# Kernel optimization log

Measured on AMD Instinct MI355X. Metric: run time of the kernel, lower is better.

Reference implementation:

```python
import jax, jax.numpy as jnp
import numpy as np

# DeformConv (RegSeg): offset conv + mask conv (sigmoid) + modulated deformable conv v2
STRIDE = 1
PAD = 1
DIL = 1
G = 1          # deformable_groups
KH, KW = 3, 3


def _conv(x, w, b):
    # standard NCHW conv, stride/pad/dilation of the module
    y = jax.lax.conv_general_dilated(
        x, w, window_strides=(STRIDE, STRIDE),
        padding=((PAD, PAD), (PAD, PAD)), rhs_dilation=(DIL, DIL),
        dimension_numbers=("NCHW", "OIHW", "NCHW"))
    return y + b[None, :, None, None]


def _deform_conv2d(x, offset, mask, w, b):
    # torchvision DeformConv2d (modulated, v2) semantics
    B, C, H, W = x.shape
    O = w.shape[0]
    K = KH * KW
    Ho = (H + 2 * PAD - DIL * (KH - 1) - 1) // STRIDE + 1
    Wo = (W + 2 * PAD - DIL * (KW - 1) - 1) // STRIDE + 1
    Cg = C // G

    # base sampling grid: p0 + p_k
    ky = jnp.repeat(jnp.arange(KH), KW) * DIL            # [K]
    kx = jnp.tile(jnp.arange(KW), KH) * DIL              # [K]
    oy = jnp.arange(Ho) * STRIDE - PAD                   # [Ho]
    ox = jnp.arange(Wo) * STRIDE - PAD                   # [Wo]
    base_y = (ky[:, None, None] + oy[None, :, None]).astype(x.dtype)  # [K,Ho,1]
    base_x = (kx[:, None, None] + ox[None, None, :]).astype(x.dtype)  # [K,1,Wo]

    off = offset.reshape(B, G, K, 2, Ho, Wo)             # channel layout: g, k, (dy,dx)
    py = base_y[None, None] + off[:, :, :, 0]            # [B,G,K,Ho,Wo]
    px = base_x[None, None] + off[:, :, :, 1]
    m = mask.reshape(B, G, K, Ho, Wo)

    imgf = x.reshape(B * G, Cg, H * W)
    y0 = jnp.floor(py).astype(jnp.int32)
    x0 = jnp.floor(px).astype(jnp.int32)
    ly = py - y0.astype(x.dtype)
    lx = px - x0.astype(x.dtype)

    def corner(iy, ix, wgt):
        # zero-padded bilinear corner: out-of-bounds corners contribute 0
        valid = (iy >= 0) & (iy < H) & (ix >= 0) & (ix < W)
        idx = (jnp.clip(iy, 0, H - 1) * W + jnp.clip(ix, 0, W - 1)).reshape(B * G, -1)
        g = jax.vmap(lambda im, ii: im[:, ii])(imgf, idx)            # [B*G,Cg,K*Ho*Wo]
        g = g.reshape(B, G, Cg, K, Ho, Wo)
        return g * (wgt * valid.astype(x.dtype))[:, :, None]          # [B,G,Cg,K,Ho,Wo]

    val = (corner(y0,     x0,     (1 - ly) * (1 - lx))
         + corner(y0,     x0 + 1, (1 - ly) * lx)
         + corner(y0 + 1, x0,     ly * (1 - lx))
         + corner(y0 + 1, x0 + 1, ly * lx))
    val = val * m[:, :, None]                                         # modulation

    wr = w.reshape(O, G, Cg, K)
    out = jnp.einsum("bgckpq,ogck->bopq", val, wr) + b[None, :, None, None]
    return out


def setup_inputs() -> dict:
    key = jax.random.key(0)
    ks = jax.random.split(key, 8)
    B, C, H, W, O = 4, 128, 96, 96, 128
    K = KH * KW
    fan = 1.0 / np.sqrt(C * K)
    return {
        "x":        jax.random.normal(ks[0], (B, C, H, W), jnp.float32),
        "x2":       jax.random.normal(ks[1], (B, C, H, W), jnp.float32),
        "offset_w": jax.random.normal(ks[2], (2 * G * K, C, KH, KW), jnp.float32) * 0.01,
        "offset_b": jax.random.normal(ks[3], (2 * G * K,), jnp.float32) * 0.01,
        "mask_w":   jax.random.normal(ks[4], (G * K, C, KH, KW), jnp.float32) * 0.05,
        "mask_b":   jnp.zeros((G * K,), jnp.float32),
        "deform_w": jax.random.normal(ks[5], (O, C, KH, KW), jnp.float32) * fan,
        "deform_b": jax.random.normal(ks[6], (O,), jnp.float32) * fan,
    }


def reference(x, x2, offset_w, offset_b, mask_w, mask_b, deform_w, deform_b):
    offset = _conv(x2, offset_w, offset_b)
    mask = jax.nn.sigmoid(_conv(x2, mask_w, mask_b))
    return _deform_conv2d(x, offset, mask, deform_w, deform_b)
```

## Files before the change

### kernel.cpp

```cpp
#include <hip/hip_runtime.h>

#define CIN   128
#define HH    96
#define WW    96
#define OUTC  128
#define HWSZ  9216
#define KK    9
#define KTOT  1152

typedef __bf16 bf16x8 __attribute__((ext_vector_type(8)));
typedef float  f32x4  __attribute__((ext_vector_type(4)));

__device__ __forceinline__ unsigned short f2bf(float f) {
  unsigned u = __builtin_bit_cast(unsigned, f);
  u += 0x7fffu + ((u >> 16) & 1u);
  return (unsigned short)(u >> 16);
}
__device__ __forceinline__ float bf2f_lo(unsigned w) {
  unsigned u = w << 16;
  return __builtin_bit_cast(float, u);
}
__device__ __forceinline__ float bf2f_hi(unsigned w) {
  unsigned u = w & 0xffff0000u;
  return __builtin_bit_cast(float, u);
}
__device__ __forceinline__ unsigned pack_bf(float v0, float v1) {
  unsigned u0 = __builtin_bit_cast(unsigned, v0) + 0x8000u;
  unsigned u1 = __builtin_bit_cast(unsigned, v1) + 0x8000u;
  return __builtin_amdgcn_perm(u1, u0, 0x07060302u);
}

#define WT2B_O 147456
#define BIAS_O 184320
#define XN_O   184384
#define X2N_O  (184384 + 4718592)

__global__ __launch_bounds__(256) void prep_all(
    const float* __restrict__ x, const float* __restrict__ x2,
    const float* __restrict__ offw, const float* __restrict__ maskw,
    const float* __restrict__ defw, const float* __restrict__ offb,
    const float* __restrict__ maskb, void* __restrict__ wsv) {
  int bid = blockIdx.x;
  int t = threadIdx.x;
  if (bid < 1152) {
    __shared__ unsigned short tile[64][138];
    int tsel = bid / 576;
    int rem = bid - tsel * 576;
    int b = rem / 144;
    int hw0 = (rem % 144) * 64;
    const float* src = tsel ? x2 : x;
    unsigned short* dst = (unsigned short*)wsv + (tsel ? X2N_O : XN_O);
    int px = t & 63, cg = t >> 6;
#pragma unroll
    for (int q = 0; q < 16; ++q) {
      int c = cg * 32 + 2 * q;
      float f0 = src[((size_t)(b * CIN + c))     * HWSZ + hw0 + px];
      float f1 = src[((size_t)(b * CIN + c + 1)) * HWSZ + hw0 + px];
      *(unsigned*)&tile[px][c] = pack_bf(f0, f1);
    }
    __syncthreads();
    unsigned* drow = (unsigned*)(dst + ((size_t)(b * HWSZ + hw0)) * 128);
#pragma unroll
    for (int k = 0; k < 16; ++k) {
      int e = t + 256 * k;
      int pxx = e >> 6, j = e & 63;
      unsigned v = *(const unsigned*)&tile[pxx][2 * j];
      drow[(size_t)pxx * 64 + j] = v;
    }
    return;
  }
  unsigned short* wtb  = (unsigned short*)wsv;
  unsigned short* wt2b = wtb + WT2B_O;
  float* bias32 = (float*)(wtb + BIAS_O);
  int idx = (bid - 1152) * 256 + t;
  if (idx < OUTC * KTOT) {
    int o = idx / KTOT, r = idx - o * KTOT;
    int c = r / KK, tap = r - c * KK;
    wtb[o * KTOT + tap * 128 + c] = f2bf(defw[idx]);
  } else if (idx < OUTC * KTOT + 32 * KTOT) {
    int j = idx - OUTC * KTOT;
    int oc = j / KTOT, r = j - oc * KTOT;
    int c = r / KK, tap = r - c * KK;
    float v = 0.f;
    if (oc < 18)      v = offw[j];
    else if (oc < 27) v = maskw[j - 18 * KTOT];
    wt2b[oc * KTOT + tap * 128 + c] = f2bf(v);
  } else if (idx < OUTC * KTOT + 32 * KTOT + 32) {
    int j = idx - OUTC * KTOT - 32 * KTOT;
    float v = 0.f;
    if (j < 18) v = offb[j]; else if (j < 27) v = maskb[j - 18];
    bias32[j] = v;
  }
}

__global__ __launch_bounds__(256, 3) void fused(
    const float* __restrict__ defb, const void* __restrict__ wsv,
    float* __restrict__ out) {
  const unsigned short* wtb  = (const unsigned short*)wsv;
  const unsigned short* wt2b = wtb + WT2B_O;
  const float* bias32 = (const float*)(wtb + BIAS_O);
  const unsigned short* xn  = wtb + XN_O;
  const unsigned short* x2n = wtb + X2N_O;

  __shared__ unsigned bw[64 * 68];
  __shared__ unsigned short val[64][136];
  __shared__ float om[32][68];
  __shared__ unsigned sidxw[KK * 4 * 64];

  int t = threadIdx.x;
  int w = t >> 6;
  int l15 = t & 15, quad = (t >> 4) & 3;
  int rb = blockIdx.x;
  int bid = (rb & 7) * 72 + (rb >> 3);
  int b = bid / 144;
  int pblk = (bid % 144) * 64;

  int phg[4], pwg[4];
#pragma unroll
  for (int G = 0; G < 4; ++G) {
    int p = pblk + w * 16 + G * 4 + quad;
    phg[G] = p / WW;
    pwg[G] = p - phg[G] * WW;
  }

  f32x4 oa0 = {0.f, 0.f, 0.f, 0.f};
  f32x4 oa1 = {0.f, 0.f, 0.f, 0.f};
  const unsigned short* x2nb = x2n + ((size_t)b * HWSZ) * 128;
  for (int tap = 0; tap < KK; ++tap) {
    int ky = tap / 3 - 1, kx = tap % 3 - 1;
    uint4 vG[4];
#pragma unroll
    for (int G = 0; G < 4; ++G) {
      int y = phg[G] + ky, xx = pwg[G] + kx;
      bool ok = ((unsigned)y < HH) && ((unsigned)xx < WW);
      int pos = ok ? (y * WW + xx) : 0;
      uint4 v = *(const uint4*)(x2nb + ((size_t)pos << 7) + l15 * 8);
      vG[G] = ok ? v : make_uint4(0u, 0u, 0u, 0u);
    }
#pragma unroll
    for (int j = 0; j < 2; ++j) {
      int cc = t + 256 * j;
      int row = cc >> 4, c16 = cc & 15;
      *(uint4*)&bw[row * 68 + c16 * 4] =
          *(const uint4*)(wt2b + (size_t)row * KTOT + tap * 128 + c16 * 8);
    }
#pragma unroll
    for (int G = 0; G < 4; ++G)
      *(uint4*)&val[w * 16 + G * 4 + quad][l15 * 8] = vG[G];
    __syncthreads();
#pragma unroll
    for (int ks = 0; ks < 4; ++ks) {
      bf16x8 af = *(const bf16x8*)&val[w * 16 + l15][ks * 32 + quad * 8];
      bf16x8 b0 = *(const bf16x8*)&bw[(size_t)l15 * 68 + ks * 16 + quad * 4];
      bf16x8 b1 = *(const bf16x8*)&bw[(size_t)(l15 + 16) * 68 + ks * 16 + quad * 4];
      oa0 = __builtin_amdgcn_mfma_f32_16x16x32_bf16(af, b0, oa0, 0, 0, 0);
      oa1 = __builtin_amdgcn_mfma_f32_16x16x32_bf16(af, b1, oa1, 0, 0, 0);
    }
    __syncthreads();
  }
#pragma unroll
  for (int nt = 0; nt < 2; ++nt) {
    f32x4 a = nt ? oa1 : oa0;
    int oc = nt * 16 + l15;
    float bia = bias32[oc];
#pragma unroll
    for (int r = 0; r < 4; ++r)
      om[oc][w * 16 + quad * 4 + r] = a[r] + bia;
  }
  __syncthreads();

  for (int e = t; e < KK * 64; e += 256) {
    int tap = e >> 6, pp = e & 63;
    int gp2 = pblk + pp;
    int h = gp2 / WW, ww_ = gp2 % WW;
    float dy = om[2 * tap][pp], dx = om[2 * tap + 1][pp];
    float mr = om[18 + tap][pp];
    float m = 1.f / (1.f + __expf(-mr));
    float py  = (float)(h + tap / 3 - 1) + dy;
    float pxx = (float)(ww_ + tap % 3 - 1) + dx;
    float y0f = floorf(py), x0f = floorf(pxx);
    int y0 = (int)y0f, x0 = (int)x0f;
    float ly = py - y0f, lx = pxx - x0f;
    int y1 = y0 + 1, x1 = x0 + 1;
    bool vy0 = (unsigned)y0 < HH, vy1 = (unsigned)y1 < HH;
    bool vx0 = (unsigned)x0 < WW, vx1 = (unsigned)x1 < WW;
    int cy0 = min(max(y0, 0), HH - 1), cy1 = min(max(y1, 0), HH - 1);
    int cx0 = min(max(x0, 0), WW - 1), cx1 = min(max(x1, 0), WW - 1);
    unsigned i00 = cy0 * WW + cx0, i01 = cy0 * WW + cx1;
    unsigned i10 = cy1 * WW + cx0, i11 = cy1 * WW + cx1;
    float w00 = (vy0 && vx0) ? m * (1.f - ly) * (1.f - lx) : 0.f;
    float w01 = (vy0 && vx1) ? m * (1.f - ly) * lx         : 0.f;
    float w10 = (vy1 && vx0) ? m * ly * (1.f - lx)         : 0.f;
    float w11 = (vy1 && vx1) ? m * ly * lx                 : 0.f;
    sidxw[(tap * 4 + 0) * 64 + pp] = i00 | ((unsigned)f2bf(w00) << 16);
    sidxw[(tap * 4 + 1) * 64 + pp] = i01 | ((unsigned)f2bf(w01) << 16);
    sidxw[(tap * 4 + 2) * 64 + pp] = i10 | ((unsigned)f2bf(w10) << 16);
    sidxw[(tap * 4 + 3) * 64 + pp] = i11 | ((unsigned)f2bf(w11) << 16);
  }
  __syncthreads();

  f32x4 acc[8];
#pragma unroll
  for (int nt = 0; nt < 8; ++nt) acc[nt] = (f32x4){0.f, 0.f, 0.f, 0.f};
  const unsigned short* xnb = xn + ((size_t)b * HWSZ) * 128;

  for (int tap = 0; tap < KK; ++tap) {
    unsigned sw[4][4];
#pragma unroll
    for (int cr = 0; cr < 4; ++cr)
#pragma unroll
      for (int G = 0; G < 4; ++G)
        sw[cr][G] = sidxw[(tap * 4 + cr) * 64 + w * 16 + G * 4 + quad];
    uint4 v[4][4];
#pragma unroll
    for (int G = 0; G < 4; ++G)
#pragma unroll
      for (int cr = 0; cr < 4; ++cr)
        v[cr][G] = *(const uint4*)(xnb + ((size_t)(sw[cr][G] & 0xffffu) << 7) + l15 * 8);
#pragma unroll
    for (int G = 0; G < 4; ++G) {
      float f[8];
#pragma unroll
      for (int j = 0; j < 8; ++j) f[j] = 0.f;
#pragma unroll
      for (int cr = 0; cr < 4; ++cr) {
        float wc = bf2f_hi(sw[cr][G]);
        const unsigned* a = (const unsigned*)&v[cr][G];
#pragma unroll
        for (int j = 0; j < 4; ++j) {
          f[2 * j]     += wc * bf2f_lo(a[j]);
          f[2 * j + 1] += wc * bf2f_hi(a[j]);
        }
      }
      unsigned od[4];
#pragma unroll
      for (int j = 0; j < 4; ++j) od[j] = pack_bf(f[2 * j], f[2 * j + 1]);
      *(uint4*)&val[w * 16 + G * 4 + quad][l15 * 8] =
          make_uint4(od[0], od[1], od[2], od[3]);
    }
#pragma unroll
    for (int j = 0; j < 4; ++j) {
      int cc = t + 256 * j;
      int row = cc >> 4, c16 = cc & 15;
      *(uint4*)&bw[row * 68 + c16 * 4] =
          *(const uint4*)(wtb + (size_t)row * KTOT + tap * 128 + c16 * 8);
    }
    __syncthreads();
    bf16x8 af[4];
#pragma unroll
    for (int ks = 0; ks < 4; ++ks)
      af[ks] = *(const bf16x8*)&val[w * 16 + l15][ks * 32 + quad * 8];
#pragma unroll
    for (int ks = 0; ks < 4; ++ks)
#pragma unroll
      for (int nt = 0; nt < 4; ++nt) {
        bf16x8 bb = *(const bf16x8*)&bw[(size_t)(nt * 16 + l15) * 68 + ks * 16 + quad * 4];
        acc[nt] = __builtin_amdgcn_mfma_f32_16x16x32_bf16(af[ks], bb, acc[nt], 0, 0, 0);
      }
    __syncthreads();
#pragma unroll
    for (int j = 0; j < 4; ++j) {
      int cc = t + 256 * j;
      int row = cc >> 4, c16 = cc & 15;
      *(uint4*)&bw[row * 68 + c16 * 4] =
          *(const uint4*)(wtb + (size_t)(64 + row) * KTOT + tap * 128 + c16 * 8);
    }
    __syncthreads();
#pragma unroll
    for (int ks = 0; ks < 4; ++ks)
#pragma unroll
      for (int nt = 0; nt < 4; ++nt) {
        bf16x8 bb = *(const bf16x8*)&bw[(size_t)(nt * 16 + l15) * 68 + ks * 16 + quad * 4];
        acc[4 + nt] = __builtin_amdgcn_mfma_f32_16x16x32_bf16(af[ks], bb, acc[4 + nt], 0, 0, 0);
      }
    __syncthreads();
  }

  for (int r = 0; r < 4; ++r) {
    f32x4 a0 = acc[2 * r], a1 = acc[2 * r + 1];
    float db0 = defb[r * 32 + l15];
    float db1 = defb[r * 32 + 16 + l15];
    if (r) __syncthreads();
#pragma unroll
    for (int reg = 0; reg < 4; ++reg) {
      om[l15]     [w * 16 + quad * 4 + reg] = a0[reg] + db0;
      om[16 + l15][w * 16 + quad * 4 + reg] = a1[reg] + db1;
    }
    __syncthreads();
    int row = t >> 4;
    int col4 = (t & 15) * 4;
#pragma unroll
    for (int hrow = 0; hrow < 2; ++hrow) {
      int rr = row + hrow * 16;
      float4 vv = *(float4*)&om[rr][col4];
      *(float4*)&out[((size_t)b * OUTC + r * 32 + rr) * HWSZ + pblk + col4] = vv;
    }
  }
}

extern "C" void kernel_launch(void* const* d_in, const int* in_sizes, int n_in,
                              void* d_out, int out_size, void* d_ws, size_t ws_size,
                              hipStream_t stream) {
  const float* x     = (const float*)d_in[0];
  const float* x2    = (const float*)d_in[1];
  const float* offw  = (const float*)d_in[2];
  const float* offb  = (const float*)d_in[3];
  const float* maskw = (const float*)d_in[4];
  const float* maskb = (const float*)d_in[5];
  const float* defw  = (const float*)d_in[6];
  const float* defb  = (const float*)d_in[7];
  float* out = (float*)d_out;

  hipLaunchKernelGGL(prep_all, dim3(1873), dim3(256), 0, stream,
                     x, x2, offw, maskw, defw, offb, maskb, d_ws);
  hipLaunchKernelGGL(fused, dim3(576), dim3(256), 0, stream, defb, d_ws, out);
}
```

Baseline: 143.7 us.

## Pipeline weight staging via global_load_lds and keep A fragments in registers

Both GEMM phases (offset/mask conv and deformable conv) are restructured. Each lane now loads its A-operand data directly in MFMA fragment layout into registers, which removes the LDS round-trip for activations. Weights are staged into a single swizzled 128x128 LDS buffer using direct global-to-LDS loads. A software pipeline issues the next tap's gathers before the current MFMAs, with manual vmcnt waits and barriers, so the output-channel halves no longer need separate passes. The hand-written waitcnt counts depend on the compiler's instruction ordering and could be fragile, and holding more data in registers may affect occupancy.

```diff
diff --git a/kernel.cpp b/kernel.cpp
--- a/kernel.cpp
+++ b/kernel.cpp
@@ -28,6 +28,11 @@
   unsigned u0 = __builtin_bit_cast(unsigned, v0) + 0x8000u;
   unsigned u1 = __builtin_bit_cast(unsigned, v1) + 0x8000u;
   return __builtin_amdgcn_perm(u1, u0, 0x07060302u);
+}
+__device__ __forceinline__ void gload16(const void* g, void* l) {
+  __builtin_amdgcn_global_load_lds(
+      (const __attribute__((address_space(1))) void*)g,
+      (__attribute__((address_space(3))) void*)l, 16, 0, 0);
 }
 
 #define WT2B_O 147456
@@ -102,8 +107,7 @@
   const unsigned short* xn  = wtb + XN_O;
   const unsigned short* x2n = wtb + X2N_O;
 
-  __shared__ unsigned bw[64 * 68];
-  __shared__ unsigned short val[64][136];
+  __shared__ unsigned short bwl[128 * 128];
   __shared__ float om[32][68];
   __shared__ unsigned sidxw[KK * 4 * 64];
 
@@ -115,49 +119,82 @@
   int b = bid / 144;
   int pblk = (bid % 144) * 64;
 
-  int phg[4], pwg[4];
-#pragma unroll
-  for (int G = 0; G < 4; ++G) {
-    int p = pblk + w * 16 + G * 4 + quad;
-    phg[G] = p / WW;
-    pwg[G] = p - phg[G] * WW;
-  }
-
+  int prow = pblk + w * 16 + l15;
+  int ph = prow / WW;
+  int pw_ = prow - ph * WW;
+
+  const unsigned short* x2nb = x2n + ((size_t)b * HWSZ) * 128;
+  const unsigned short* xnb  = xn  + ((size_t)b * HWSZ) * 128;
+
+  uint4 va[4]; unsigned okm;
+  auto issueA1 = [&](int tap) {
+    int ky = tap / 3 - 1, kx = tap % 3 - 1;
+    int y = ph + ky, xx = pw_ + kx;
+    bool ok = ((unsigned)y < HH) && ((unsigned)xx < WW);
+    int pos = ok ? (y * WW + xx) : 0;
+    const unsigned short* p = x2nb + ((size_t)pos << 7) + quad * 8;
+    va[0] = *(const uint4*)(p);
+    va[1] = *(const uint4*)(p + 32);
+    va[2] = *(const uint4*)(p + 64);
+    va[3] = *(const uint4*)(p + 96);
+    okm = ok ? 0xffffffffu : 0u;
+  };
+  auto maskA = [&](bf16x8* af) {
+#pragma unroll
+    for (int ks = 0; ks < 4; ++ks) {
+      uint4 m = va[ks];
+      m.x &= okm; m.y &= okm; m.z &= okm; m.w &= okm;
+      af[ks] = __builtin_bit_cast(bf16x8, m);
+    }
+  };
+  auto stage1 = [&](int tap) {
+#pragma unroll
+    for (int i = 0; i < 2; ++i) {
+      int r = (w * 2 + i) * 4 + quad;
+      const unsigned short* src =
+          wt2b + (size_t)r * KTOT + tap * 128 + ((l15 ^ (r & 7)) << 3);
+      gload16(src, (char*)bwl + ((w * 2 + i) << 10));
+    }
+  };
   f32x4 oa0 = {0.f, 0.f, 0.f, 0.f};
   f32x4 oa1 = {0.f, 0.f, 0.f, 0.f};
-  const unsigned short* x2nb = x2n + ((size_t)b * HWSZ) * 128;
-  for (int tap = 0; tap < KK; ++tap) {
-    int ky = tap / 3 - 1, kx = tap % 3 - 1;
-    uint4 vG[4];
-#pragma unroll
-    for (int G = 0; G < 4; ++G) {
-      int y = phg[G] + ky, xx = pwg[G] + kx;
-      bool ok = ((unsigned)y < HH) && ((unsigned)xx < WW);
-      int pos = ok ? (y * WW + xx) : 0;
-      uint4 v = *(const uint4*)(x2nb + ((size_t)pos << 7) + l15 * 8);
-      vG[G] = ok ? v : make_uint4(0u, 0u, 0u, 0u);
-    }
-#pragma unroll
-    for (int j = 0; j < 2; ++j) {
-      int cc = t + 256 * j;
-      int row = cc >> 4, c16 = cc & 15;
-      *(uint4*)&bw[row * 68 + c16 * 4] =
-          *(const uint4*)(wt2b + (size_t)row * KTOT + tap * 128 + c16 * 8);
-    }
-#pragma unroll
-    for (int G = 0; G < 4; ++G)
-      *(uint4*)&val[w * 16 + G * 4 + quad][l15 * 8] = vG[G];
-    __syncthreads();
+  auto mfma1 = [&](bf16x8* af) {
 #pragma unroll
     for (int ks = 0; ks < 4; ++ks) {
-      bf16x8 af = *(const bf16x8*)&val[w * 16 + l15][ks * 32 + quad * 8];
-      bf16x8 b0 = *(const bf16x8*)&bw[(size_t)l15 * 68 + ks * 16 + quad * 4];
-      bf16x8 b1 = *(const bf16x8*)&bw[(size_t)(l15 + 16) * 68 + ks * 16 + quad * 4];
-      oa0 = __builtin_amdgcn_mfma_f32_16x16x32_bf16(af, b0, oa0, 0, 0, 0);
-      oa1 = __builtin_amdgcn_mfma_f32_16x16x32_bf16(af, b1, oa1, 0, 0, 0);
-    }
-    __syncthreads();
-  }
+      int cs = ((ks * 4 + quad) ^ (l15 & 7)) << 4;
+      bf16x8 b0 = *(const bf16x8*)((const char*)bwl + l15 * 256 + cs);
+      bf16x8 b1 = *(const bf16x8*)((const char*)bwl + (l15 + 16) * 256 + cs);
+      oa0 = __builtin_amdgcn_mfma_f32_16x16x32_bf16(af[ks], b0, oa0, 0, 0, 0);
+      oa1 = __builtin_amdgcn_mfma_f32_16x16x32_bf16(af[ks], b1, oa1, 0, 0, 0);
+    }
+  };
+
+  issueA1(0);
+  asm volatile("" ::: "memory");
+  stage1(0);
+  asm volatile("" ::: "memory");
+#pragma unroll 1
+  for (int tap = 0; tap < 8; ++tap) {
+    bf16x8 af[4]; maskA(af);
+    issueA1(tap + 1);
+    asm volatile("s_waitcnt vmcnt(4)" ::: "memory");
+    __builtin_amdgcn_s_barrier();
+    asm volatile("" ::: "memory");
+    mfma1(af);
+    asm volatile("s_waitcnt lgkmcnt(0)" ::: "memory");
+    __builtin_amdgcn_s_barrier();
+    asm volatile("" ::: "memory");
+    stage1(tap + 1);
+    asm volatile("" ::: "memory");
+  }
+  {
+    bf16x8 af[4]; maskA(af);
+    asm volatile("s_waitcnt vmcnt(0)" ::: "memory");
+    __builtin_amdgcn_s_barrier();
+    asm volatile("" ::: "memory");
+    mfma1(af);
+  }
+
 #pragma unroll
   for (int nt = 0; nt < 2; ++nt) {
     f32x4 a = nt ? oa1 : oa0;
@@ -202,30 +239,32 @@
   f32x4 acc[8];
 #pragma unroll
   for (int nt = 0; nt < 8; ++nt) acc[nt] = (f32x4){0.f, 0.f, 0.f, 0.f};
-  const unsigned short* xnb = xn + ((size_t)b * HWSZ) * 128;
-
-  for (int tap = 0; tap < KK; ++tap) {
-    unsigned sw[4][4];
+
+  uint4 gv[4][4]; unsigned swv[4];
+  auto loadG = [&](int tap) {
 #pragma unroll
     for (int cr = 0; cr < 4; ++cr)
-#pragma unroll
-      for (int G = 0; G < 4; ++G)
-        sw[cr][G] = sidxw[(tap * 4 + cr) * 64 + w * 16 + G * 4 + quad];
-    uint4 v[4][4];
-#pragma unroll
-    for (int G = 0; G < 4; ++G)
-#pragma unroll
-      for (int cr = 0; cr < 4; ++cr)
-        v[cr][G] = *(const uint4*)(xnb + ((size_t)(sw[cr][G] & 0xffffu) << 7) + l15 * 8);
-#pragma unroll
-    for (int G = 0; G < 4; ++G) {
+      swv[cr] = sidxw[(tap * 4 + cr) * 64 + w * 16 + l15];
+#pragma unroll
+    for (int cr = 0; cr < 4; ++cr) {
+      const unsigned short* p =
+          xnb + ((size_t)(swv[cr] & 0xffffu) << 7) + quad * 8;
+      gv[cr][0] = *(const uint4*)(p);
+      gv[cr][1] = *(const uint4*)(p + 32);
+      gv[cr][2] = *(const uint4*)(p + 64);
+      gv[cr][3] = *(const uint4*)(p + 96);
+    }
+  };
+  auto combine = [&](bf16x8* af) {
+#pragma unroll
+    for (int ks = 0; ks < 4; ++ks) {
       float f[8];
 #pragma unroll
       for (int j = 0; j < 8; ++j) f[j] = 0.f;
 #pragma unroll
       for (int cr = 0; cr < 4; ++cr) {
-        float wc = bf2f_hi(sw[cr][G]);
-        const unsigned* a = (const unsigned*)&v[cr][G];
+        float wc = bf2f_hi(swv[cr]);
+        const unsigned* a = (const unsigned*)&gv[cr][ks];
 #pragma unroll
         for (int j = 0; j < 4; ++j) {
           f[2 * j]     += wc * bf2f_lo(a[j]);
@@ -235,45 +274,57 @@
       unsigned od[4];
 #pragma unroll
       for (int j = 0; j < 4; ++j) od[j] = pack_bf(f[2 * j], f[2 * j + 1]);
-      *(uint4*)&val[w * 16 + G * 4 + quad][l15 * 8] =
-          make_uint4(od[0], od[1], od[2], od[3]);
-    }
-#pragma unroll
-    for (int j = 0; j < 4; ++j) {
-      int cc = t + 256 * j;
-      int row = cc >> 4, c16 = cc & 15;
-      *(uint4*)&bw[row * 68 + c16 * 4] =
-          *(const uint4*)(wtb + (size_t)row * KTOT + tap * 128 + c16 * 8);
-    }
-    __syncthreads();
-    bf16x8 af[4];
-#pragma unroll
-    for (int ks = 0; ks < 4; ++ks)
-      af[ks] = *(const bf16x8*)&val[w * 16 + l15][ks * 32 + quad * 8];
-#pragma unroll
-    for (int ks = 0; ks < 4; ++ks)
-#pragma unroll
-      for (int nt = 0; nt < 4; ++nt) {
-        bf16x8 bb = *(const bf16x8*)&bw[(size_t)(nt * 16 + l15) * 68 + ks * 16 + quad * 4];
-        acc[nt] = __builtin_amdgcn_mfma_f32_16x16x32_bf16(af[ks], bb, acc[nt], 0, 0, 0);
+      uint4 u = make_uint4(od[0], od[1], od[2], od[3]);
+      af[ks] = __builtin_bit_cast(bf16x8, u);
+    }
+  };
+  auto stage3 = [&](int tap) {
+#pragma unroll
+    for (int i = 0; i < 8; ++i) {
+      int r = (w * 8 + i) * 4 + quad;
+      const unsigned short* src =
+          wtb + (size_t)r * KTOT + tap * 128 + ((l15 ^ (r & 7)) << 3);
+      gload16(src, (char*)bwl + ((w * 8 + i) << 10));
+    }
+  };
+  auto mfma3 = [&](bf16x8* af) {
+#pragma unroll
+    for (int ks = 0; ks < 4; ++ks) {
+      int cs = ((ks * 4 + quad) ^ (l15 & 7)) << 4;
+#pragma unroll
+      for (int nt = 0; nt < 8; ++nt) {
+        bf16x8 bb =
+            *(const bf16x8*)((const char*)bwl + (nt * 16 + l15) * 256 + cs);
+        acc[nt] = __builtin_amdgcn_mfma_f32_16x16x32_bf16(af[ks], bb, acc[nt],
+                                                          0, 0, 0);
       }
-    __syncthreads();
-#pragma unroll
-    for (int j = 0; j < 4; ++j) {
-      int cc = t + 256 * j;
-      int row = cc >> 4, c16 = cc & 15;
-      *(uint4*)&bw[row * 68 + c16 * 4] =
-          *(const uint4*)(wtb + (size_t)(64 + row) * KTOT + tap * 128 + c16 * 8);
-    }
-    __syncthreads();
-#pragma unroll
-    for (int ks = 0; ks < 4; ++ks)
-#pragma unroll
-      for (int nt = 0; nt < 4; ++nt) {
-        bf16x8 bb = *(const bf16x8*)&bw[(size_t)(nt * 16 + l15) * 68 + ks * 16 + quad * 4];
-        acc[4 + nt] = __builtin_amdgcn_mfma_f32_16x16x32_bf16(af[ks], bb, acc[4 + nt], 0, 0, 0);
-      }
-    __syncthreads();
+    }
+  };
+
+  loadG(0);
+  asm volatile("" ::: "memory");
+  stage3(0);
+  asm volatile("" ::: "memory");
+#pragma unroll 1
+  for (int tap = 0; tap < 8; ++tap) {
+    bf16x8 af[4]; combine(af);
+    loadG(tap + 1);
+    asm volatile("s_waitcnt vmcnt(16)" ::: "memory");
+    __builtin_amdgcn_s_barrier();
+    asm volatile("" ::: "memory");
+    mfma3(af);
+    asm volatile("s_waitcnt lgkmcnt(0)" ::: "memory");
+    __builtin_amdgcn_s_barrier();
+    asm volatile("" ::: "memory");
+    stage3(tap + 1);
+    asm volatile("" ::: "memory");
+  }
+  {
+    bf16x8 af[4]; combine(af);
+    asm volatile("s_waitcnt vmcnt(0)" ::: "memory");
+    __builtin_amdgcn_s_barrier();
+    asm volatile("" ::: "memory");
+    mfma3(af);
   }
 
   for (int r = 0; r < 4; ++r) {
```

New measurement: 173.9 us. +21.0%, slower.
